# Kernel optimization log

Measured on AMD Instinct MI355X. Metric: run time of the kernel, lower is better.

## Reference

```python
import jax, jax.numpy as jnp
import numpy as np

R = 5                       # kernels_radius
D = 2 * R + 1               # kernels_diameter
KERNELS_DESC = [
    {"weight": 0.9, "xy": 6.0, "image": 0.1},
    {"weight": 0.1, "xy": 6.0},
]


def _unfold(t, r):
    """torch F.unfold with padding=r, stride=1 -> [N, C, D, D, H, W]."""
    N, C, H, W = t.shape
    d = 2 * r + 1
    tp = jnp.pad(t, ((0, 0), (0, 0), (r, r), (r, r)))
    # fixed small loop over D*D kernel offsets (121), not over data dims
    pats = jnp.stack(
        [tp[:, :, i:i + H, j:j + W] for i in range(d) for j in range(d)],
        axis=2,
    )
    return pats.reshape(N, C, d, d, H, W)


def reference(x, y_hat):
    N, _, H, W = x.shape
    dt = x.dtype
    # xy coordinate feature [N, 2, H, W]: (col index, row index)
    cols = jnp.broadcast_to(jnp.arange(W, dtype=dt)[None, :], (H, W))
    rows = jnp.broadcast_to(jnp.arange(H, dtype=dt)[:, None], (H, W))
    xy = jnp.broadcast_to(jnp.stack([cols, rows], 0)[None], (N, 2, H, W))

    kernels = jnp.zeros((N, 1, D, D, H, W), dtype=dt)
    for desc in KERNELS_DESC:
        feats = []
        for modality, sigma in desc.items():
            if modality == 'weight':
                continue
            f = xy if modality == 'xy' else x
            feats.append(f / sigma)
        features = jnp.concatenate(feats, axis=1)          # [N, c, H, W]
        k = _unfold(features, R)                           # [N, c, D, D, H, W]
        k = k - k[:, :, R, R][:, :, None, None]            # diff to window center
        k = jnp.exp((-0.5 * k ** 2).sum(axis=1, keepdims=True))
        k = k.at[:, :, R, R].set(0.0)                      # zero self-affinity
        kernels = kernels + desc['weight'] * k

    Cy = y_hat.shape[1]
    yu = _unfold(y_hat, R)                                  # [N, Cy, D, D, H, W]
    prod = (kernels * yu).reshape(N, Cy, D * D, H, W).sum(axis=2)
    loss = kernels.sum() - (prod * y_hat).sum()
    denom = jnp.asarray(N * H * W, dtype=dt)
    return loss / denom


def setup_inputs() -> dict:
    key = jax.random.key(0)
    k1, k2 = jax.random.split(key)
    x = jax.random.normal(k1, (4, 3, 128, 128), dtype=jnp.float32)
    y_hat = jax.random.uniform(k2, (4, 21, 128, 128), dtype=jnp.float32)
    return {"x": x, "y_hat": y_hat}
```

## Files before the change

### kernel.cpp

```cpp
#include <hip/hip_runtime.h>

constexpr int IMG_H = 128;
constexpr int IMG_W = 128;
constexpr int N_IMG = 4;
constexpr int CXCH = 3;
constexpr int CYCH = 21;
constexpr int RAD = 5;
constexpr int DIA = 11;
constexpr int TILE_H = 8;
constexpr int TILE_W = 16;
constexpr int PT_H = TILE_H + 2 * RAD;
constexpr int PT_W = TILE_W + 2 * RAD;
constexpr int NPIX = PT_H * PT_W;
constexpr int NTHREADS = TILE_H * TILE_W;
constexpr int HW = IMG_H * IMG_W;

__global__ __launch_bounds__(NTHREADS)
void gcrf_kernel(const float* __restrict__ x, const float* __restrict__ y,
                 float* __restrict__ out) {
    __shared__ __align__(16) float sy[NPIX * 20];
    __shared__ __align__(16) float sx[NPIX * 4];
    __shared__ float s_exy[DIA * DIA];
    __shared__ float s_red[NTHREADS / 64];

    const int tid = threadIdx.x;
    const int n = blockIdx.z;
    const int h0 = blockIdx.y * TILE_H;
    const int w0 = blockIdx.x * TILE_W;

    const float* xb = x + (size_t)n * CXCH * HW;
    const float* yb = y + (size_t)n * CYCH * HW;

    if (tid < DIA * DIA) {
        int di = tid / DIA - RAD, dj = tid % DIA - RAD;
        s_exy[tid] = __expf(-0.5f * (float)(di * di + dj * dj) * (1.0f / 36.0f));
    }

    for (int p = tid; p < NPIX; p += NTHREADS) {
        int ti = p / PT_W, tj = p - ti * PT_W;
        int gh = h0 + ti - RAD, gw = w0 + tj - RAD;
        bool inb = ((unsigned)gh < (unsigned)IMG_H) && ((unsigned)gw < (unsigned)IMG_W);
        int gofs = gh * IMG_W + gw;
        float v[CYCH];
        #pragma unroll
        for (int c = 0; c < CYCH; c++) v[c] = inb ? yb[c * HW + gofs] : 0.0f;
        float xv[CXCH];
        #pragma unroll
        for (int c = 0; c < CXCH; c++) xv[c] = inb ? xb[c * HW + gofs] : 0.0f;
        #pragma unroll
        for (int q = 0; q < 5; q++) {
            *(float4*)&sy[p * 20 + q * 4] =
                make_float4(v[q * 4 + 0], v[q * 4 + 1], v[q * 4 + 2], v[q * 4 + 3]);
        }
        *(float4*)&sx[p * 4] = make_float4(xv[0], xv[1], xv[2], v[20]);
    }
    __syncthreads();

    const int tx = tid & (TILE_W - 1);
    const int ty = tid >> 4;
    const int h = h0 + ty, w = w0 + tx;
    const int cp = (ty + RAD) * PT_W + (tx + RAD);

    const float4 cx4 = *(const float4*)&sx[cp * 4];
    float yc[20];
    #pragma unroll
    for (int q = 0; q < 5; q++) {
        float4 t = *(const float4*)&sy[cp * 20 + q * 4];
        yc[q * 4 + 0] = t.x; yc[q * 4 + 1] = t.y;
        yc[q * 4 + 2] = t.z; yc[q * 4 + 3] = t.w;
    }

    int i0 = max(0, RAD - h), i1 = min(DIA - 1, IMG_H - 1 - h + RAD);
    int j0 = max(0, RAD - w), j1 = min(DIA - 1, IMG_W - 1 - w + RAD);
    int n_oob = DIA * DIA - (i1 - i0 + 1) * (j1 - j0 + 1);
    float acc = 0.0f;
    if (n_oob > 0) {
        float oxy = (float)(h * h + w * w) * (1.0f / 36.0f);
        float s2c = cx4.x * cx4.x + cx4.y * cx4.y + cx4.z * cx4.z;
        float kvo = __expf(-0.5f * oxy) * (0.9f * __expf(-50.0f * s2c) + 0.1f);
        acc = (float)n_oob * kvo;
    }

    float accp = 0.0f;
    auto pair_term = [&](int i, int j) {
        int p = cp + (i - RAD) * PT_W + (j - RAD);
        float4 xq = *(const float4*)&sx[p * 4];
        float dot = xq.w * cx4.w;
        #pragma unroll
        for (int q = 0; q < 5; q++) {
            float4 t = *(const float4*)&sy[p * 20 + q * 4];
            dot += t.x * yc[q * 4 + 0] + t.y * yc[q * 4 + 1] +
                   t.z * yc[q * 4 + 2] + t.w * yc[q * 4 + 3];
        }
        float d0 = xq.x - cx4.x, d1 = xq.y - cx4.y, d2 = xq.z - cx4.z;
        float s2 = d0 * d0 + d1 * d1 + d2 * d2;
        int hh2 = h + (i - RAD);
        int ww2 = w + (j - RAD);
        bool inb = (hh2 < IMG_H) && ((unsigned)ww2 < (unsigned)IMG_W);
        float e1 = inb ? s_exy[i * DIA + j] : 0.0f;
        float kv = e1 * (0.9f * __expf(-50.0f * s2) + 0.1f);
        accp += kv * (1.0f - dot);
    };

    #pragma unroll
    for (int j = RAD + 1; j < DIA; j++) pair_term(RAD, j);
    for (int i = RAD + 1; i < DIA; i++) {
        #pragma unroll
        for (int j = 0; j < DIA; j++) pair_term(i, j);
    }

    float total = acc + 2.0f * accp;

    #pragma unroll
    for (int s = 32; s > 0; s >>= 1) total += __shfl_down(total, s, 64);
    if ((tid & 63) == 0) s_red[tid >> 6] = total;
    __syncthreads();
    if (tid == 0) {
        float bs = 0.0f;
        #pragma unroll
        for (int wv = 0; wv < NTHREADS / 64; wv++) bs += s_red[wv];
        atomicAdd(out, bs * (1.0f / (float)(N_IMG * HW)));
    }
}

extern "C" void kernel_launch(void* const* d_in, const int* in_sizes, int n_in,
                              void* d_out, int out_size, void* d_ws, size_t ws_size,
                              hipStream_t stream) {
    const float* x = (const float*)d_in[0];
    const float* y = (const float*)d_in[1];
    float* out = (float*)d_out;
    hipMemsetAsync(out, 0, sizeof(float), stream);
    dim3 grid(IMG_W / TILE_W, IMG_H / TILE_H, N_IMG);
    gcrf_kernel<<<grid, NTHREADS, 0, stream>>>(x, y, out);
}
```

Baseline: 81.27 us.

## Split each pixel's 60 neighbor pairs across four thread groups

The block grows from 128 to 512 threads, and each of four thread groups handles 15 of the 60 symmetric neighbor pairs for the same pixel. Pair offsets and spatial weights now come from small shared lookup tables instead of a nested loop. The goal is more parallelism and latency hiding, since the grid has only 512 blocks of 128 threads. The trade-off is that each group reloads the 21-channel center values and shares the same shared-memory tile, and the launch bound asks for 4 blocks per CU, which limits registers.

```diff
diff --git a/kernel.cpp b/kernel.cpp
--- a/kernel.cpp
+++ b/kernel.cpp
@@ -12,15 +12,20 @@
 constexpr int PT_H = TILE_H + 2 * RAD;
 constexpr int PT_W = TILE_W + 2 * RAD;
 constexpr int NPIX = PT_H * PT_W;
-constexpr int NTHREADS = TILE_H * TILE_W;
+constexpr int NPIXT = TILE_H * TILE_W;
+constexpr int NGROUP = 4;
+constexpr int NTHREADS = NPIXT * NGROUP;
+constexpr int NPAIR = 60;
+constexpr int PPG = NPAIR / NGROUP;
 constexpr int HW = IMG_H * IMG_W;
 
-__global__ __launch_bounds__(NTHREADS)
+__global__ __launch_bounds__(NTHREADS, 4)
 void gcrf_kernel(const float* __restrict__ x, const float* __restrict__ y,
                  float* __restrict__ out) {
     __shared__ __align__(16) float sy[NPIX * 20];
     __shared__ __align__(16) float sx[NPIX * 4];
-    __shared__ float s_exy[DIA * DIA];
+    __shared__ int   s_pk[NPAIR];
+    __shared__ float s_e1[NPAIR];
     __shared__ float s_red[NTHREADS / 64];
 
     const int tid = threadIdx.x;
@@ -31,9 +36,12 @@
     const float* xb = x + (size_t)n * CXCH * HW;
     const float* yb = y + (size_t)n * CYCH * HW;
 
-    if (tid < DIA * DIA) {
-        int di = tid / DIA - RAD, dj = tid % DIA - RAD;
-        s_exy[tid] = __expf(-0.5f * (float)(di * di + dj * dj) * (1.0f / 36.0f));
+    if (tid < NPAIR) {
+        int di, dj;
+        if (tid < 5) { di = 0; dj = tid + 1; }
+        else         { int m = tid - 5; di = 1 + m / 11; dj = m % 11 - 5; }
+        s_pk[tid] = (di << 8) | (dj + 8);
+        s_e1[tid] = __expf(-0.5f * (float)(di * di + dj * dj) * (1.0f / 36.0f));
     }
 
     for (int p = tid; p < NPIX; p += NTHREADS) {
@@ -56,8 +64,10 @@
     }
     __syncthreads();
 
-    const int tx = tid & (TILE_W - 1);
-    const int ty = tid >> 4;
+    const int g = tid >> 7;
+    const int pix = tid & (NPIXT - 1);
+    const int tx = pix & (TILE_W - 1);
+    const int ty = pix >> 4;
     const int h = h0 + ty, w = w0 + tx;
     const int cp = (ty + RAD) * PT_W + (tx + RAD);
 
@@ -70,43 +80,41 @@
         yc[q * 4 + 2] = t.z; yc[q * 4 + 3] = t.w;
     }
 
-    int i0 = max(0, RAD - h), i1 = min(DIA - 1, IMG_H - 1 - h + RAD);
-    int j0 = max(0, RAD - w), j1 = min(DIA - 1, IMG_W - 1 - w + RAD);
-    int n_oob = DIA * DIA - (i1 - i0 + 1) * (j1 - j0 + 1);
     float acc = 0.0f;
-    if (n_oob > 0) {
-        float oxy = (float)(h * h + w * w) * (1.0f / 36.0f);
-        float s2c = cx4.x * cx4.x + cx4.y * cx4.y + cx4.z * cx4.z;
-        float kvo = __expf(-0.5f * oxy) * (0.9f * __expf(-50.0f * s2c) + 0.1f);
-        acc = (float)n_oob * kvo;
+    if (g == 0) {
+        int i0 = max(0, RAD - h), i1 = min(DIA - 1, IMG_H - 1 - h + RAD);
+        int j0 = max(0, RAD - w), j1 = min(DIA - 1, IMG_W - 1 - w + RAD);
+        int n_oob = DIA * DIA - (i1 - i0 + 1) * (j1 - j0 + 1);
+        if (n_oob > 0) {
+            float oxy = (float)(h * h + w * w) * (1.0f / 36.0f);
+            float s2c = cx4.x * cx4.x + cx4.y * cx4.y + cx4.z * cx4.z;
+            float kvo = __expf(-0.5f * oxy) * (0.9f * __expf(-50.0f * s2c) + 0.1f);
+            acc = (float)n_oob * kvo;
+        }
     }
 
     float accp = 0.0f;
-    auto pair_term = [&](int i, int j) {
-        int p = cp + (i - RAD) * PT_W + (j - RAD);
+    #pragma unroll
+    for (int t = 0; t < PPG; t++) {
+        int k = g * PPG + t;
+        int pk = s_pk[k];
+        float e1 = s_e1[k];
+        int di = pk >> 8, dj = (pk & 255) - 8;
+        int p = cp + di * PT_W + dj;
         float4 xq = *(const float4*)&sx[p * 4];
         float dot = xq.w * cx4.w;
         #pragma unroll
         for (int q = 0; q < 5; q++) {
-            float4 t = *(const float4*)&sy[p * 20 + q * 4];
-            dot += t.x * yc[q * 4 + 0] + t.y * yc[q * 4 + 1] +
-                   t.z * yc[q * 4 + 2] + t.w * yc[q * 4 + 3];
+            float4 tt = *(const float4*)&sy[p * 20 + q * 4];
+            dot += tt.x * yc[q * 4 + 0] + tt.y * yc[q * 4 + 1] +
+                   tt.z * yc[q * 4 + 2] + tt.w * yc[q * 4 + 3];
         }
         float d0 = xq.x - cx4.x, d1 = xq.y - cx4.y, d2 = xq.z - cx4.z;
         float s2 = d0 * d0 + d1 * d1 + d2 * d2;
-        int hh2 = h + (i - RAD);
-        int ww2 = w + (j - RAD);
-        bool inb = (hh2 < IMG_H) && ((unsigned)ww2 < (unsigned)IMG_W);
-        float e1 = inb ? s_exy[i * DIA + j] : 0.0f;
-        float kv = e1 * (0.9f * __expf(-50.0f * s2) + 0.1f);
+        bool inb = ((h + di) < IMG_H) && ((unsigned)(w + dj) < (unsigned)IMG_W);
+        float e = inb ? e1 : 0.0f;
+        float kv = e * (0.9f * __expf(-50.0f * s2) + 0.1f);
         accp += kv * (1.0f - dot);
-    };
-
-    #pragma unroll
-    for (int j = RAD + 1; j < DIA; j++) pair_term(RAD, j);
-    for (int i = RAD + 1; i < DIA; i++) {
-        #pragma unroll
-        for (int j = 0; j < DIA; j++) pair_term(i, j);
     }
 
     float total = acc + 2.0f * accp;
```

Result: faster. 76.90 us (-5.4%).
